# Kernel tuning notes

Hardware: AMD Instinct MI355X
Metric: run time of the kernel (lower is better)

The kernel has to match this reference:

```python
import jax, jax.numpy as jnp
import numpy as np

NEG = jnp.float32(-1e9)


def setup_inputs() -> dict:
    key = jax.random.key(0)
    ks = jax.random.split(key, 8)
    B, S, D = 8, 2048, 1024
    scale = 1.0 / np.sqrt(D)
    return {
        "xQ": jax.random.normal(ks[0], (B, S, D), jnp.float32),
        "xK": jax.random.normal(ks[1], (B, S, D), jnp.float32),
        "xV": jax.random.normal(ks[2], (B, S, D), jnp.float32),
        "padding_mask": jax.random.randint(ks[3], (B, S), 0, 2, jnp.int32),
        "casual_mask": jnp.ones((B, S), jnp.int32),
        "W_q": jax.random.normal(ks[4], (D, D), jnp.float32) * scale,
        "b_q": jnp.zeros((D,), jnp.float32),
        "W_k": jax.random.normal(ks[5], (D, D), jnp.float32) * scale,
        "b_k": jnp.zeros((D,), jnp.float32),
        "W_v": jax.random.normal(ks[6], (D, D), jnp.float32) * scale,
        "b_v": jnp.zeros((D,), jnp.float32),
    }


def reference(xQ, xK, xV, padding_mask, casual_mask, W_q, b_q, W_k, b_k, W_v, b_v):
    # Linear projections (torch nn.Linear: x @ W.T + b)
    Q = jnp.einsum('bsd,ed->bse', xQ, W_q) + b_q
    K = jnp.einsum('bsd,ed->bse', xK, W_k) + b_k
    V = jnp.einsum('bsd,ed->bse', xV, W_v) + b_v

    # Raw logits (note: original code applies NO 1/sqrt(dk) scaling)
    QKT = jnp.einsum('bqd,bkd->bqk', Q, K)  # [B, Sq, Sk]

    # Additive padding mask: -1e9 on padded key positions
    pad = jnp.where(padding_mask[:, None, :] == 0, NEG, jnp.float32(0.0))
    # Additive causal mask: -1e9 above the diagonal
    Sq, Sk = QKT.shape[1], QKT.shape[2]
    caus = jnp.where(
        jnp.tril(jnp.ones((Sq, Sk), dtype=bool)), jnp.float32(0.0), NEG
    )[None, :, :]
    QKT = QKT + pad + caus

    S = jax.nn.softmax(QKT, axis=-1)
    return jnp.einsum('bqk,bkd->bqd', S, V)
```

## Files before the change

### kernel.cpp

```cpp
#include <hip/hip_runtime.h>

typedef __attribute__((ext_vector_type(4))) float f4;
typedef __attribute__((ext_vector_type(4))) float f32x4;
typedef _Float16 half8 __attribute__((ext_vector_type(8)));

#define DEVI static __device__ __forceinline__

DEVI void gload_lds16(const void* g, void* l) {
  __builtin_amdgcn_global_load_lds(
      (const __attribute__((address_space(1))) void*)g,
      (__attribute__((address_space(3))) void*)l, 16, 0, 0);
}

DEVI unsigned int pack2(_Float16 a, _Float16 b) {
  unsigned short ua = __builtin_bit_cast(unsigned short, a);
  unsigned short ub = __builtin_bit_cast(unsigned short, b);
  return (unsigned int)ua | ((unsigned int)ub << 16);
}

DEVI int xcd_swz(int id, int n) {
  int q = n >> 3, r = n & 7;
  int x = id & 7, c = id >> 3;
  return (x < r ? x * (q + 1) : r * (q + 1) + (x - r) * q) + c;
}

#define FENCED_BARRIER()                \
  __builtin_amdgcn_sched_barrier(0);    \
  __builtin_amdgcn_s_barrier();         \
  __builtin_amdgcn_sched_barrier(0);

__global__ __launch_bounds__(256) void cvt_plain(const float* __restrict__ X,
                                                 _Float16* __restrict__ H,
                                                 int n4) {
  int i = blockIdx.x * 256 + threadIdx.x;
  const int stride = gridDim.x * 256;
  typedef _Float16 half4v __attribute__((ext_vector_type(4)));
  for (; i < n4; i += stride) {
    f4 x = ((const f4*)X)[i];
    half4v h;
#pragma unroll
    for (int j = 0; j < 4; ++j) h[j] = (_Float16)x[j];
    ((half4v*)H)[i] = h;
  }
}

template <int DUP>
__global__ __launch_bounds__(256) void cvt_wide(const float* __restrict__ X,
                                                _Float16* __restrict__ H,
                                                int n4) {
  int i = blockIdx.x * 256 + threadIdx.x;
  const int stride = gridDim.x * 256;
  for (; i < n4; i += stride) {
    f4 x = ((const f4*)X)[i];
    half8 o;
#pragma unroll
    for (int j = 0; j < 4; ++j) {
      _Float16 h = (_Float16)x[j];
      o[2 * j] = h;
      o[2 * j + 1] = DUP ? h : (_Float16)(x[j] - (float)h);
    }
    ((half8*)H)[i] = o;
  }
}

template <int AR, int BR>
DEVI void core(const _Float16* __restrict__ A0, const _Float16* __restrict__ B0,
               int lda, int ldb, int NS, _Float16* lds, f32x4 (&acc)[4][4]) {
  constexpr int WN = BR / 64;
  constexpr int ACH = AR * 32;
  constexpr int CHUNK = (AR + BR) * 32;
  const int tid = threadIdx.x;
  const int w = tid >> 6, lane = tid & 63;
  const int wm = w / WN, wn = w % WN;
  const int r16 = lane & 15, kg = lane >> 4;

  auto STAGE = [&](int t, int buf) {
    _Float16* base = lds + buf * CHUNK;
#pragma unroll
    for (int j = 0; j < AR / 128; ++j) {
      int g = j * 512 + tid;
      int row = g >> 2, c = g & 3;
      int cs = (c ^ (row >> 1)) & 3;
      gload_lds16(A0 + (size_t)row * lda + t * 32 + cs * 8,
                  base + (j * 512 + w * 64) * 8);
    }
    _Float16* bb = base + ACH;
#pragma unroll
    for (int j = 0; j < BR / 128; ++j) {
      int g = j * 512 + tid;
      int row = g >> 2, c = g & 3;
      int cs = (c ^ (row >> 1)) & 3;
      gload_lds16(B0 + (size_t)row * ldb + t * 32 + cs * 8,
                  bb + (j * 512 + w * 64) * 8);
    }
  };

  auto COMPUTE = [&](int buf) {
    const _Float16* la = lds + buf * CHUNK;
    const _Float16* lb = la + ACH;
    half8 a[4], b[4];
#pragma unroll
    for (int mi = 0; mi < 4; ++mi) {
      int row = wm * 64 + mi * 16 + r16;
      a[mi] = *(const half8*)(la + row * 32 + (((kg ^ (row >> 1)) & 3) * 8));
    }
#pragma unroll
    for (int ni = 0; ni < 4; ++ni) {
      int row = wn * 64 + ni * 16 + r16;
      b[ni] = *(const half8*)(lb + row * 32 + (((kg ^ (row >> 1)) & 3) * 8));
    }
    __builtin_amdgcn_s_setprio(1);
#pragma unroll
    for (int mi = 0; mi < 4; ++mi)
#pragma unroll
      for (int ni = 0; ni < 4; ++ni)
        acc[mi][ni] = __builtin_amdgcn_mfma_f32_16x16x32_f16(
            a[mi], b[ni], acc[mi][ni], 0, 0, 0);
    __builtin_amdgcn_s_setprio(0);
  };

  STAGE(0, 0);
  STAGE(1, 1);
  int t = 0;
  for (; t < NS - 1; ++t) {
    asm volatile("s_waitcnt vmcnt(3)" ::: "memory");
    FENCED_BARRIER();
    if (t + 2 < NS) STAGE(t + 2, (t + 2) % 3);
    COMPUTE(t % 3);
  }
  asm volatile("s_waitcnt vmcnt(0)" ::: "memory");
  FENCED_BARRIER();
  COMPUTE(t % 3);
}

DEVI void acc_zero(f32x4 (&acc)[4][4]) {
#pragma unroll
  for (int i = 0; i < 4; ++i)
#pragma unroll
    for (int j = 0; j < 4; ++j) acc[i][j] = (f32x4)0.0f;
}

template <int OUTMODE>
__global__ __launch_bounds__(512, 4) void proj_eng(
    const _Float16* __restrict__ Xi, const _Float16* __restrict__ Wd,
    const float* __restrict__ bias, unsigned int* __restrict__ OutU) {
  extern __shared__ _Float16 lds[];
  const int id = xcd_swz(blockIdx.x, gridDim.x);
  const int m0 = (id >> 3) * 256, n0 = (id & 7) * 128;
  f32x4 acc[4][4];
  acc_zero(acc);
  core<256, 128>(Xi + (size_t)m0 * 2048, Wd + (size_t)n0 * 2048, 2048, 2048,
                 64, lds, acc);
  const int tid = threadIdx.x;
  const int w = tid >> 6, lane = tid & 63;
  const int wm = w >> 1, wn = w & 1;
  const int r16 = lane & 15, kg = lane >> 4;
  float bcol[4];
#pragma unroll
  for (int ni = 0; ni < 4; ++ni) bcol[ni] = bias[n0 + wn * 64 + ni * 16 + r16];
#pragma unroll
  for (int mi = 0; mi < 4; ++mi) {
    int row = m0 + wm * 64 + mi * 16 + kg * 4;
#pragma unroll
    for (int ni = 0; ni < 4; ++ni) {
      int col = n0 + wn * 64 + ni * 16 + r16;
#pragma unroll
      for (int j = 0; j < 4; ++j) {
        float v = acc[mi][ni][j] + bcol[ni];
        _Float16 h = (_Float16)v;
        _Float16 x2 = OUTMODE ? h : (_Float16)(v - (float)h);
        OutU[(size_t)(row + j) * 1024 + col] = pack2(h, x2);
      }
    }
  }
}

__global__ __launch_bounds__(512, 4) void proj_eng_v(
    const _Float16* __restrict__ X, const _Float16* __restrict__ Wh,
    const float* __restrict__ bias, _Float16* __restrict__ Vt) {
  extern __shared__ _Float16 lds[];
  const int id = xcd_swz(blockIdx.x, gridDim.x);
  const int m0 = (id >> 3) * 256, n0 = (id & 7) * 128;
  f32x4 acc[4][4];
  acc_zero(acc);
  core<256, 128>(X + (size_t)m0 * 1024, Wh + (size_t)n0 * 1024, 1024, 1024, 32,
                 lds, acc);
  const int tid = threadIdx.x;
  const int w = tid >> 6, lane = tid & 63;
  const int wm = w >> 1, wn = w & 1;
  const int r16 = lane & 15, kg = lane >> 4;
  float bcol[4];
#pragma unroll
  for (int ni = 0; ni < 4; ++ni) bcol[ni] = bias[n0 + wn * 64 + ni * 16 + r16];
  __syncthreads();
  _Float16(*T)[256] = (_Float16(*)[256])lds;
#pragma unroll
  for (int mi = 0; mi < 4; ++mi) {
    int ml = wm * 64 + mi * 16 + kg * 4;
#pragma unroll
    for (int ni = 0; ni < 4; ++ni) {
      int nl = wn * 64 + ni * 16 + r16;
#pragma unroll
      for (int j = 0; j < 4; ++j)
        T[nl][ml + j] = (_Float16)(acc[mi][ni][j] + bcol[ni]);
    }
  }
  __syncthreads();
  const int b = m0 >> 11;
  const int s0 = m0 & 2047;
#pragma unroll
  for (int r = 0; r < 8; ++r) {
    int flat = tid + r * 512;
    int n = flat >> 5, c = flat & 31;
    half8 v = *(const half8*)&T[n][c * 8];
    *(half8*)(Vt + (size_t)b * (1024 * 2048) + (size_t)(n0 + n) * 2048 + s0 +
              c * 8) = v;
  }
}

__global__ __launch_bounds__(512, 4) void qk_eng(
    const _Float16* __restrict__ Qi, const _Float16* __restrict__ Kd,
    float* __restrict__ Lg, int bbase) {
  extern __shared__ _Float16 lds[];
  const int id = xcd_swz(blockIdx.x, gridDim.x);
  const int y = id / 72;
  int t = id % 72;
  int qt = 0, base = 0;
  while (t >= base + (qt >> 1) + 1) { base += (qt >> 1) + 1; ++qt; }
  const int kt = t - base;
  const int b = bbase + y;
  f32x4 acc[4][4];
  acc_zero(acc);
  core<128, 256>(Qi + ((size_t)b * 2048 + qt * 128) * 2048,
                 Kd + ((size_t)b * 2048 + kt * 256) * 2048, 2048, 2048, 64,
                 lds, acc);
  const int tid = threadIdx.x;
  const int w = tid >> 6, lane = tid & 63;
  const int wm = w >> 2, wn = w & 3;
  const int r16 = lane & 15, kg = lane >> 4;
  float* L = Lg + (size_t)y * (2048 * 2048);
#pragma unroll
  for (int mi = 0; mi < 4; ++mi) {
    int row = qt * 128 + wm * 64 + mi * 16 + kg * 4;
#pragma unroll
    for (int ni = 0; ni < 4; ++ni) {
      int col = kt * 256 + wn * 64 + ni * 16 + r16;
#pragma unroll
      for (int j = 0; j < 4; ++j)
        L[(size_t)(row + j) * 2048 + col] = acc[mi][ni][j];
    }
  }
}

__global__ __launch_bounds__(512, 4) void pv_eng(
    const float* __restrict__ Lg, const _Float16* __restrict__ Vt,
    float* __restrict__ Out, int bbase) {
  extern __shared__ _Float16 lds[];
  const int id = xcd_swz(blockIdx.x, gridDim.x);
  const int y = id >> 6;
  const int qt = (id & 63) >> 2, nt = id & 3;
  const int b = bbase + y;
  const _Float16* P = (const _Float16*)(Lg + (size_t)y * (2048 * 2048));
  f32x4 acc[4][4];
  acc_zero(acc);
  core<128, 256>(P + (size_t)(qt * 128) * 4096,
                 Vt + (size_t)b * (1024 * 2048) + (size_t)(nt * 256) * 2048,
                 4096, 2048, ((qt >> 1) + 1) * 8, lds, acc);
  const int tid = threadIdx.x;
  const int w = tid >> 6, lane = tid & 63;
  const int wm = w >> 2, wn = w & 3;
  const int r16 = lane & 15, kg = lane >> 4;
#pragma unroll
  for (int mi = 0; mi < 4; ++mi) {
    int row = qt * 128 + wm * 64 + mi * 16 + kg * 4;
#pragma unroll
    for (int ni = 0; ni < 4; ++ni) {
      int col = nt * 256 + wn * 64 + ni * 16 + r16;
#pragma unroll
      for (int j = 0; j < 4; ++j)
        Out[(size_t)(b * 2048 + row + j) * 1024 + col] = acc[mi][ni][j];
    }
  }
}

template <int OUTMODE>
__global__ __launch_bounds__(256) void proj_legacy(
    const float* __restrict__ X, const float* __restrict__ W,
    const float* __restrict__ bias, unsigned int* __restrict__ OutU) {
  __shared__ struct {
    float As[128][36];
    float Bs[128][36];
  } u;
  const int tid = threadIdx.x;
  const int lane = tid & 63, w = tid >> 6;
  const int wm = w >> 1, wn = w & 1;
  const int r16 = lane & 15, kg = lane >> 4;
  const int m0 = blockIdx.y * 128, n0 = blockIdx.x * 128;
  f32x4 acc[4][4];
  acc_zero(acc);
  f4 ra[4], rb[4];
  auto LOAD = [&](int kt) {
#pragma unroll
    for (int r = 0; r < 4; ++r) {
      int flat = tid + r * 256;
      int row = flat >> 3, c = flat & 7;
      ra[r] = *(const f4*)(X + (size_t)(m0 + row) * 1024 + kt * 32 + c * 4);
      rb[r] = *(const f4*)(W + (size_t)(n0 + row) * 1024 + kt * 32 + c * 4);
    }
  };
  LOAD(0);
  for (int kt = 0; kt < 32; ++kt) {
    __syncthreads();
#pragma unroll
    for (int r = 0; r < 4; ++r) {
      int flat = tid + r * 256;
      int row = flat >> 3, c = flat & 7;
      *(f4*)&u.As[row][c * 4] = ra[r];
      *(f4*)&u.Bs[row][c * 4] = rb[r];
    }
    __syncthreads();
    if (kt + 1 < 32) LOAD(kt + 1);
    half8 ah[4], al[4], bh[4];
#pragma unroll
    for (int mi = 0; mi < 4; ++mi) {
      const float* p = &u.As[wm * 64 + mi * 16 + r16][kg * 8];
      f4 x0 = *(const f4*)p, x1 = *(const f4*)(p + 4);
      half8 h, l;
#pragma unroll
      for (int j = 0; j < 4; ++j) {
        h[j] = (_Float16)x0[j];
        h[j + 4] = (_Float16)x1[j];
        l[j] = (_Float16)(x0[j] - (float)h[j]);
        l[j + 4] = (_Float16)(x1[j] - (float)h[j + 4]);
      }
      ah[mi] = h;
      al[mi] = l;
    }
#pragma unroll
    for (int ni = 0; ni < 4; ++ni) {
      const float* p = &u.Bs[wn * 64 + ni * 16 + r16][kg * 8];
      f4 x0 = *(const f4*)p, x1 = *(const f4*)(p + 4);
      half8 h;
#pragma unroll
      for (int j = 0; j < 4; ++j) {
        h[j] = (_Float16)x0[j];
        h[j + 4] = (_Float16)x1[j];
      }
      bh[ni] = h;
    }
#pragma unroll
    for (int mi = 0; mi < 4; ++mi)
#pragma unroll
      for (int ni = 0; ni < 4; ++ni) {
        acc[mi][ni] = __builtin_amdgcn_mfma_f32_16x16x32_f16(
            ah[mi], bh[ni], acc[mi][ni], 0, 0, 0);
        acc[mi][ni] = __builtin_amdgcn_mfma_f32_16x16x32_f16(
            al[mi], bh[ni], acc[mi][ni], 0, 0, 0);
      }
  }
  float bcol[4];
#pragma unroll
  for (int ni = 0; ni < 4; ++ni) bcol[ni] = bias[n0 + wn * 64 + ni * 16 + r16];
#pragma unroll
  for (int mi = 0; mi < 4; ++mi) {
    int row = m0 + wm * 64 + mi * 16 + kg * 4;
#pragma unroll
    for (int ni = 0; ni < 4; ++ni) {
      int col = n0 + wn * 64 + ni * 16 + r16;
#pragma unroll
      for (int j = 0; j < 4; ++j) {
        float v = acc[mi][ni][j] + bcol[ni];
        _Float16 h = (_Float16)v;
        _Float16 x2 = OUTMODE ? h : (_Float16)(v - (float)h);
        OutU[(size_t)(row + j) * 1024 + col] = pack2(h, x2);
      }
    }
  }
}

__global__ __launch_bounds__(256) void softmax_kernel(
    float* __restrict__ Lg, const int* __restrict__ pad, int bbase) {
  const int q = blockIdx.x;
  const int y = blockIdx.y;
  const int b = bbase + y;
  const int tid = threadIdx.x;
  float* row = Lg + (size_t)y * (2048 * 2048) + (size_t)q * 2048;
  _Float16* prow = (_Float16*)row;
  const int* pb = pad + (size_t)b * 2048;
  const int kend = ((q >> 8) + 1) << 8;
  float v[8];
  int nv = 0;
  float mx = -3.0e38f;
  for (int k = tid; k <= q; k += 256) {
    float l = row[k];
    if (pb[k] == 0) l += -1.0e9f;
    v[nv++] = l;
    mx = fmaxf(mx, l);
  }
  __shared__ float red[4];
  for (int o = 32; o; o >>= 1) mx = fmaxf(mx, __shfl_xor(mx, o));
  if ((tid & 63) == 0) red[tid >> 6] = mx;
  __syncthreads();
  mx = fmaxf(fmaxf(red[0], red[1]), fmaxf(red[2], red[3]));
  __syncthreads();
  float s = 0.f;
  for (int i = 0; i < nv; ++i) s += expf(v[i] - mx);
  for (int o = 32; o; o >>= 1) s += __shfl_xor(s, o);
  if ((tid & 63) == 0) red[tid >> 6] = s;
  __syncthreads();
  s = red[0] + red[1] + red[2] + red[3];
  const float inv = 1.0f / s;
  int i = 0;
  for (int k = tid; k <= q; k += 256) {
    prow[k] = (_Float16)(expf(v[i] - mx) * inv);
    ++i;
  }
  for (int k = q + 1 + tid; k < kend; k += 256) prow[k] = (_Float16)0.0f;
}

__global__ __launch_bounds__(512) void fix_f(const int* __restrict__ pad,
                                             int* __restrict__ fb) {
  const int b = threadIdx.x >> 6, k = threadIdx.x & 63;
  unsigned long long m = __ballot(pad[b * 2048 + k] != 0);
  if (k == 0) fb[b] = m ? (__ffsll((long long)m) - 1) : 64;
}

__global__ __launch_bounds__(256) void fix_qrow2(
    const float* __restrict__ xQ, const float* __restrict__ Wq,
    const float* __restrict__ bq, const int* __restrict__ fb,
    float* __restrict__ Qrow) {
  const int b = blockIdx.y;
  const int f = fb[b];
  const int tid = threadIdx.x;
  const int e = blockIdx.x * 16 + (tid >> 4);
  const int l16 = tid & 15;
  __shared__ float xq[1024];
  for (int q = 0; q < f; ++q) {
    *(f4*)&xq[tid * 4] = ((const f4*)(xQ + (size_t)(b * 2048 + q) * 1024))[tid];
    __syncthreads();
    float a = 0.f;
#pragma unroll
    for (int it = 0; it < 16; ++it) {
      int d = l16 * 4 + it * 64;
      f4 ww = *(const f4*)(Wq + (size_t)e * 1024 + d);
      a += xq[d] * ww[0] + xq[d + 1] * ww[1] + xq[d + 2] * ww[2] +
           xq[d + 3] * ww[3];
    }
    for (int o = 8; o; o >>= 1) a += __shfl_xor(a, o);
    if (l16 == 0) Qrow[((size_t)b * 64 + q) * 1024 + e] = a + bq[e];
    __syncthreads();
  }
}

__global__ __launch_bounds__(256) void fix_qb0(const float* __restrict__ bk,
                                               const int* __restrict__ fb,
                                               const float* __restrict__ Qrow,
                                               float* __restrict__ qb0) {
  const int q = blockIdx.x, b = blockIdx.y;
  if (q >= fb[b]) return;
  const int tid = threadIdx.x;
  const float* qr = Qrow + ((size_t)b * 64 + q) * 1024;
  float p = 0.f;
  for (int e = tid; e < 1024; e += 256) p += qr[e] * bk[e];
  __shared__ float red[4];
  for (int o = 32; o; o >>= 1) p += __shfl_xor(p, o);
  if ((tid & 63) == 0) red[tid >> 6] = p;
  __syncthreads();
  if (tid == 0) qb0[b * 64 + q] = red[0] + red[1] + red[2] + red[3];
}

__global__ __launch_bounds__(256) void fix_g2(const float* __restrict__ Wk,
                                              const int* __restrict__ fb,
                                              const float* __restrict__ Qrow,
                                              float* __restrict__ Gpart) {
  const int b = blockIdx.y;
  const int f = fb[b];
  const int tid = threadIdx.x;
  const int ddblk = blockIdx.x & 3, es = blockIdx.x >> 2;
  const int dd = ddblk * 256 + tid;
  __shared__ float qc[128];
  for (int q = 0; q < f; ++q) {
    if (tid < 32)
      *(f4*)&qc[tid * 4] =
          ((const f4*)(Qrow + ((size_t)b * 64 + q) * 1024 + es * 128))[tid];
    __syncthreads();
    float g = 0.f;
    for (int e = 0; e < 128; ++e)
      g += qc[e] * Wk[(size_t)(es * 128 + e) * 1024 + dd];
    Gpart[(((size_t)es * 8 + b) * 64 + q) * 1024 + dd] = g;
    __syncthreads();
  }
}

__global__ __launch_bounds__(256) void fix_logit2(
    const float* __restrict__ xK, const int* __restrict__ pad,
    const int* __restrict__ fb, const float* __restrict__ Gpart,
    const float* __restrict__ qb0, float* __restrict__ lrow) {
  const int b = blockIdx.y;
  const int f = fb[b];
  const int tid = threadIdx.x;
  const int k = blockIdx.x * 16 + (tid >> 4);
  const int l16 = tid & 15;
  __shared__ float Gs[1024];
  for (int q = 0; q < f; ++q) {
    f4 s = (f4)0.0f;
#pragma unroll
    for (int es = 0; es < 8; ++es)
      s += ((const f4*)(Gpart + (((size_t)es * 8 + b) * 64 + q) * 1024))[tid];
    *(f4*)&Gs[tid * 4] = s;
    __syncthreads();
    float a = 0.f;
#pragma unroll
    for (int it = 0; it < 16; ++it) {
      int d = l16 * 4 + it * 64;
      f4 x = *(const f4*)(xK + (size_t)(b * 2048 + k) * 1024 + d);
      a += x[0] * Gs[d] + x[1] * Gs[d + 1] + x[2] * Gs[d + 2] +
           x[3] * Gs[d + 3];
    }
    for (int o = 8; o; o >>= 1) a += __shfl_xor(a, o);
    if (l16 == 0) {
      float l = a + qb0[b * 64 + q];
      if (pad[b * 2048 + k] == 0) l += -1.0e9f;
      if (k > q) l += -1.0e9f;
      lrow[((size_t)b * 64 + q) * 2048 + k] = l;
    }
    __syncthreads();
  }
}

__global__ __launch_bounds__(256) void fix_sm(const int* __restrict__ fb,
                                              float* __restrict__ lrow,
                                              float* __restrict__ srow) {
  const int q = blockIdx.x, b = blockIdx.y;
  if (q >= fb[b]) return;
  const int tid = threadIdx.x;
  float* row = lrow + ((size_t)b * 64 + q) * 2048;
  float v[8];
  float mx = -3.0e38f;
#pragma unroll
  for (int i = 0; i < 8; ++i) {
    v[i] = row[tid + i * 256];
    mx = fmaxf(mx, v[i]);
  }
  __shared__ float red[4];
  for (int o = 32; o; o >>= 1) mx = fmaxf(mx, __shfl_xor(mx, o));
  if ((tid & 63) == 0) red[tid >> 6] = mx;
  __syncthreads();
  mx = fmaxf(fmaxf(red[0], red[1]), fmaxf(red[2], red[3]));
  __syncthreads();
  float s = 0.f;
#pragma unroll
  for (int i = 0; i < 8; ++i) {
    v[i] = expf(v[i] - mx);
    s += v[i];
  }
#pragma unroll
  for (int i = 0; i < 8; ++i) row[tid + i * 256] = v[i];
  for (int o = 32; o; o >>= 1) s += __shfl_xor(s, o);
  if ((tid & 63) == 0) red[tid >> 6] = s;
  __syncthreads();
  if (tid == 0) srow[b * 64 + q] = red[0] + red[1] + red[2] + red[3];
}

__global__ __launch_bounds__(256) void fix_pv2(
    const _Float16* __restrict__ Vt, const int* __restrict__ fb,
    const float* __restrict__ lrow, const float* __restrict__ srow,
    float* __restrict__ Out) {
  const int b = blockIdx.y;
  const int f = fb[b];
  const int tid = threadIdx.x;
  const int d = blockIdx.x * 16 + (tid >> 4);
  const int l16 = tid & 15;
  __shared__ float ps[2048];
  for (int q = 0; q < f; ++q) {
    const f4* src = (const f4*)(lrow + ((size_t)b * 64 + q) * 2048);
    *(f4*)&ps[tid * 8] = src[tid * 2];
    *(f4*)&ps[tid * 8 + 4] = src[tid * 2 + 1];
    __syncthreads();
    float o = 0.f;
#pragma unroll
    for (int it = 0; it < 16; ++it) {
      int k = l16 * 8 + it * 128;
      half8 vv = *(const half8*)(Vt + (size_t)b * (1024 * 2048) +
                                 (size_t)d * 2048 + k);
      o += (float)vv[0] * ps[k] + (float)vv[1] * ps[k + 1] +
           (float)vv[2] * ps[k + 2] + (float)vv[3] * ps[k + 3] +
           (float)vv[4] * ps[k + 4] + (float)vv[5] * ps[k + 5] +
           (float)vv[6] * ps[k + 6] + (float)vv[7] * ps[k + 7];
    }
    for (int of = 8; of; of >>= 1) o += __shfl_xor(o, of);
    if (l16 == 0)
      Out[(size_t)(b * 2048 + q) * 1024 + d] = o * (1.0f / srow[b * 64 + q]);
    __syncthreads();
  }
}

extern "C" void kernel_launch(void* const* d_in, const int* in_sizes, int n_in,
                              void* d_out, int out_size, void* d_ws,
                              size_t ws_size, hipStream_t stream) {
  const float* xQ = (const float*)d_in[0];
  const float* xK = (const float*)d_in[1];
  const float* xV = (const float*)d_in[2];
  const int* pad = (const int*)d_in[3];
  const float* Wq = (const float*)d_in[5];
  const float* bq = (const float*)d_in[6];
  const float* Wk = (const float*)d_in[7];
  const float* bk = (const float*)d_in[8];
  const float* Wv = (const float*)d_in[9];
  const float* bv = (const float*)d_in[10];
  float* Out = (float*)d_out;

  const size_t MB = (size_t)1 << 20;
  char* wsb = (char*)d_ws;
  _Float16* Qi = (_Float16*)(wsb);
  _Float16* Kd = (_Float16*)(wsb + 64 * MB);
  _Float16* Vt = (_Float16*)(wsb + 128 * MB);
  float* Lg = (float*)(wsb + 160 * MB);

  size_t avail = (ws_size > 160 * MB) ? ws_size - 160 * MB : 0;
  int G = (int)(avail / (16 * MB));
  if (G > 8) G = 8;
  if (G < 1) G = 1;

  const int SMEM = 73728;
  (void)hipFuncSetAttribute((const void*)&proj_eng<0>,
                            hipFuncAttributeMaxDynamicSharedMemorySize, SMEM);
  (void)hipFuncSetAttribute((const void*)&proj_eng<1>,
                            hipFuncAttributeMaxDynamicSharedMemorySize, SMEM);
  (void)hipFuncSetAttribute((const void*)&proj_eng_v,
                            hipFuncAttributeMaxDynamicSharedMemorySize, SMEM);
  (void)hipFuncSetAttribute((const void*)&qk_eng,
                            hipFuncAttributeMaxDynamicSharedMemorySize, SMEM);
  (void)hipFuncSetAttribute((const void*)&pv_eng,
                            hipFuncAttributeMaxDynamicSharedMemorySize, SMEM);

  dim3 blk(256), eblk(512);
  const bool fast = (ws_size >= 228 * MB);

  {
    _Float16* sX = (_Float16*)(wsb);
    _Float16* sW = (_Float16*)(wsb + 32 * MB);
    cvt_plain<<<dim3(2048), blk, 0, stream>>>(xV, sX, 4194304);
    cvt_plain<<<dim3(1024), blk, 0, stream>>>(Wv, sW, 262144);
    proj_eng_v<<<dim3(512), eblk, SMEM, stream>>>(sX, sW, bv, Vt);
  }
  if (fast) {
    _Float16* XiK = (_Float16*)(wsb);
    _Float16* WdK = (_Float16*)(wsb + 160 * MB);
    cvt_wide<0><<<dim3(2048), blk, 0, stream>>>(xK, XiK, 4194304);
    cvt_wide<1><<<dim3(1024), blk, 0, stream>>>(Wk, WdK, 262144);
    proj_eng<1><<<dim3(512), eblk, SMEM, stream>>>(XiK, WdK, bk,
                                                   (unsigned int*)Kd);
    _Float16* XiQ = (_Float16*)(wsb + 160 * MB);
    _Float16* WdQ = (_Float16*)(wsb + 224 * MB);
    cvt_wide<0><<<dim3(2048), blk, 0, stream>>>(xQ, XiQ, 4194304);
    cvt_wide<1><<<dim3(1024), blk, 0, stream>>>(Wq, WdQ, 262144);
    proj_eng<0><<<dim3(512), eblk, SMEM, stream>>>(XiQ, WdQ, bq,
                                                   (unsigned int*)Qi);
  } else {
    proj_legacy<1><<<dim3(8, 128), blk, 0, stream>>>(xK, Wk, bk,
                                                     (unsigned int*)Kd);
    proj_legacy<0><<<dim3(8, 128), blk, 0, stream>>>(xQ, Wq, bq,
                                                     (unsigned int*)Qi);
  }

  for (int bbase = 0; bbase < 8; bbase += G) {
    int nb = (8 - bbase < G) ? (8 - bbase) : G;
    qk_eng<<<dim3(72 * nb), eblk, SMEM, stream>>>(Qi, Kd, Lg, bbase);
    softmax_kernel<<<dim3(2048, nb), blk, 0, stream>>>(Lg, pad, bbase);
    pv_eng<<<dim3(64 * nb), eblk, SMEM, stream>>>(Lg, Vt, Out, bbase);
  }

  int* fb = (int*)(wsb);
  float* qb0 = (float*)(wsb + 4 * 1024);
  float* srow = (float*)(wsb + 8 * 1024);
  float* Qrow = (float*)(wsb + 1 * MB);
  float* Gpart = (float*)(wsb + 4 * MB);
  float* lrow = (float*)(wsb + 20 * MB);

  fix_f<<<dim3(1), dim3(512), 0, stream>>>(pad, fb);
  fix_qrow2<<<dim3(64, 8), blk, 0, stream>>>(xQ, Wq, bq, fb, Qrow);
  fix_qb0<<<dim3(64, 8), blk, 0, stream>>>(bk, fb, Qrow, qb0);
  fix_g2<<<dim3(32, 8), blk, 0, stream>>>(Wk, fb, Qrow, Gpart);
  fix_logit2<<<dim3(128, 8), blk, 0, stream>>>(xK, pad, fb, Gpart, qb0, lrow);
  fix_sm<<<dim3(64, 8), blk, 0, stream>>>(fb, lrow, srow);
  fix_pv2<<<dim3(64, 8), blk, 0, stream>>>(Vt, fb, lrow, srow, Out);
}
```

Baseline: 603.3 us.

## Fuse fp32-to-fp16 activation conversion into projections and split Q/K hi-lo buffers

Projection kernels now read fp32 activations directly, convert them to fp16 in registers and write them to LDS, which removes the separate activation conversion passes and their workspace traffic. Weights are split into separate hi and lo fp16 arrays that are multiplied separately. Q is likewise stored as separate hi and lo arrays, while K is stored hi-only. The QK and PV kernels are retiled into smaller tiles (64-row Q tiles, 128-column PV tiles) with more blocks for better load balance across the causal triangle. The legacy fallback path is removed. Risks include lower occupancy (launch bounds 512,2), a serialised register-staged A pipeline in the projections, and the inner products now running a different number of split-precision MFMA passes.

```diff
diff --git a/kernel.cpp b/kernel.cpp
--- a/kernel.cpp
+++ b/kernel.cpp
@@ -12,12 +12,6 @@
       (__attribute__((address_space(3))) void*)l, 16, 0, 0);
 }
 
-DEVI unsigned int pack2(_Float16 a, _Float16 b) {
-  unsigned short ua = __builtin_bit_cast(unsigned short, a);
-  unsigned short ub = __builtin_bit_cast(unsigned short, b);
-  return (unsigned int)ua | ((unsigned int)ub << 16);
-}
-
 DEVI int xcd_swz(int id, int n) {
   int q = n >> 3, r = n & 7;
   int x = id & 7, c = id >> 3;
@@ -28,6 +22,8 @@
   __builtin_amdgcn_sched_barrier(0);    \
   __builtin_amdgcn_s_barrier();         \
   __builtin_amdgcn_sched_barrier(0);
+
+#define SWZ(kgv, rowv) ((((kgv) ^ ((rowv) >> 1)) & 3) * 8)
 
 __global__ __launch_bounds__(256) void cvt_plain(const float* __restrict__ X,
                                                  _Float16* __restrict__ H,
@@ -44,207 +40,291 @@
   }
 }
 
-template <int DUP>
-__global__ __launch_bounds__(256) void cvt_wide(const float* __restrict__ X,
-                                                _Float16* __restrict__ H,
-                                                int n4) {
+__global__ __launch_bounds__(256) void cvt_split(const float* __restrict__ X,
+                                                 _Float16* __restrict__ H,
+                                                 _Float16* __restrict__ L,
+                                                 int n4) {
   int i = blockIdx.x * 256 + threadIdx.x;
   const int stride = gridDim.x * 256;
+  typedef _Float16 half4v __attribute__((ext_vector_type(4)));
   for (; i < n4; i += stride) {
     f4 x = ((const f4*)X)[i];
-    half8 o;
+    half4v h, l;
 #pragma unroll
     for (int j = 0; j < 4; ++j) {
-      _Float16 h = (_Float16)x[j];
-      o[2 * j] = h;
-      o[2 * j + 1] = DUP ? h : (_Float16)(x[j] - (float)h);
-    }
-    ((half8*)H)[i] = o;
-  }
-}
-
-template <int AR, int BR>
-DEVI void core(const _Float16* __restrict__ A0, const _Float16* __restrict__ B0,
-               int lda, int ldb, int NS, _Float16* lds, f32x4 (&acc)[4][4]) {
-  constexpr int WN = BR / 64;
-  constexpr int ACH = AR * 32;
-  constexpr int CHUNK = (AR + BR) * 32;
+      h[j] = (_Float16)x[j];
+      l[j] = (_Float16)(x[j] - (float)h[j]);
+    }
+    ((half4v*)H)[i] = h;
+    ((half4v*)L)[i] = l;
+  }
+}
+
+DEVI void acc_zero44(f32x4 (&acc)[4][4]) {
+#pragma unroll
+  for (int i = 0; i < 4; ++i)
+#pragma unroll
+    for (int j = 0; j < 4; ++j) acc[i][j] = (f32x4)0.0f;
+}
+DEVI void acc_zero42(f32x4 (&acc)[4][2]) {
+#pragma unroll
+  for (int i = 0; i < 4; ++i)
+#pragma unroll
+    for (int j = 0; j < 2; ++j) acc[i][j] = (f32x4)0.0f;
+}
+
+template <int WSPLIT, int OUTMODE>
+__global__ __launch_bounds__(512, 2) void proj_fused(
+    const float* __restrict__ X, const _Float16* __restrict__ Wh,
+    const _Float16* __restrict__ Wl, const float* __restrict__ bias,
+    _Float16* __restrict__ OutHi, _Float16* __restrict__ OutLo,
+    _Float16* __restrict__ VtOut) {
+  extern __shared__ _Float16 lds[];
+  constexpr int ACH = 256 * 32;
+  constexpr int BCH = 128 * 32;
+  constexpr int CHUNK = ACH + BCH * (1 + WSPLIT);
+  const int id = xcd_swz(blockIdx.x, gridDim.x);
+  const int m0 = (id >> 3) * 256, n0 = (id & 7) * 128;
+  const float* A = X + (size_t)m0 * 1024;
+  const _Float16* B0 = Wh + (size_t)n0 * 1024;
+  const _Float16* B1 = Wl + (size_t)n0 * 1024;
   const int tid = threadIdx.x;
   const int w = tid >> 6, lane = tid & 63;
-  const int wm = w / WN, wn = w % WN;
+  const int wm = w >> 1, wn = w & 1;
   const int r16 = lane & 15, kg = lane >> 4;
-
-  auto STAGE = [&](int t, int buf) {
-    _Float16* base = lds + buf * CHUNK;
-#pragma unroll
-    for (int j = 0; j < AR / 128; ++j) {
-      int g = j * 512 + tid;
+  f32x4 acc[4][4];
+  acc_zero44(acc);
+  f4 ra[4];
+
+  auto ALOAD = [&](int t) {
+#pragma unroll
+    for (int j = 0; j < 2; ++j) {
+      int g = tid + j * 512;
       int row = g >> 2, c = g & 3;
-      int cs = (c ^ (row >> 1)) & 3;
-      gload_lds16(A0 + (size_t)row * lda + t * 32 + cs * 8,
-                  base + (j * 512 + w * 64) * 8);
-    }
-    _Float16* bb = base + ACH;
-#pragma unroll
-    for (int j = 0; j < BR / 128; ++j) {
-      int g = j * 512 + tid;
+      const float* src = A + (size_t)row * 1024 + t * 32 + c * 8;
+      ra[2 * j] = *(const f4*)src;
+      ra[2 * j + 1] = *(const f4*)(src + 4);
+    }
+  };
+  auto AWRITE = [&](int buf) {
+    _Float16* ab = lds + buf * CHUNK;
+#pragma unroll
+    for (int j = 0; j < 2; ++j) {
+      int g = tid + j * 512;
       int row = g >> 2, c = g & 3;
-      int cs = (c ^ (row >> 1)) & 3;
-      gload_lds16(B0 + (size_t)row * ldb + t * 32 + cs * 8,
-                  bb + (j * 512 + w * 64) * 8);
+      half8 h;
+#pragma unroll
+      for (int e = 0; e < 4; ++e) {
+        h[e] = (_Float16)ra[2 * j][e];
+        h[e + 4] = (_Float16)ra[2 * j + 1][e];
+      }
+      *(half8*)(ab + (size_t)row * 32 + SWZ(c, row)) = h;
     }
   };
-
+  auto WLOAD = [&](int t, int buf) {
+    _Float16* bb = lds + buf * CHUNK + ACH;
+    int row = tid >> 2, c = tid & 3;
+    int cs = (c ^ (row >> 1)) & 3;
+    gload_lds16(B0 + (size_t)row * 1024 + t * 32 + cs * 8, bb + tid * 8);
+    if (WSPLIT)
+      gload_lds16(B1 + (size_t)row * 1024 + t * 32 + cs * 8,
+                  bb + BCH + tid * 8);
+  };
   auto COMPUTE = [&](int buf) {
     const _Float16* la = lds + buf * CHUNK;
     const _Float16* lb = la + ACH;
-    half8 a[4], b[4];
+    half8 a[4], b0f[4], b1f[4];
 #pragma unroll
     for (int mi = 0; mi < 4; ++mi) {
       int row = wm * 64 + mi * 16 + r16;
-      a[mi] = *(const half8*)(la + row * 32 + (((kg ^ (row >> 1)) & 3) * 8));
+      a[mi] = *(const half8*)(la + row * 32 + SWZ(kg, row));
     }
 #pragma unroll
     for (int ni = 0; ni < 4; ++ni) {
       int row = wn * 64 + ni * 16 + r16;
-      b[ni] = *(const half8*)(lb + row * 32 + (((kg ^ (row >> 1)) & 3) * 8));
+      int off = row * 32 + SWZ(kg, row);
+      b0f[ni] = *(const half8*)(lb + off);
+      if (WSPLIT) b1f[ni] = *(const half8*)(lb + BCH + off);
     }
     __builtin_amdgcn_s_setprio(1);
 #pragma unroll
     for (int mi = 0; mi < 4; ++mi)
 #pragma unroll
-      for (int ni = 0; ni < 4; ++ni)
+      for (int ni = 0; ni < 4; ++ni) {
         acc[mi][ni] = __builtin_amdgcn_mfma_f32_16x16x32_f16(
-            a[mi], b[ni], acc[mi][ni], 0, 0, 0);
+            a[mi], b0f[ni], acc[mi][ni], 0, 0, 0);
+        if (WSPLIT)
+          acc[mi][ni] = __builtin_amdgcn_mfma_f32_16x16x32_f16(
+              a[mi], b1f[ni], acc[mi][ni], 0, 0, 0);
+      }
     __builtin_amdgcn_s_setprio(0);
   };
 
+  const int NS = 32;
+  WLOAD(0, 0);
+  ALOAD(0);
+  asm volatile("s_waitcnt vmcnt(0)" ::: "memory");
+  __builtin_amdgcn_sched_barrier(0);
+  AWRITE(0);
+  asm volatile("s_waitcnt lgkmcnt(0)" ::: "memory");
+  FENCED_BARRIER();
+  for (int t = 0; t < NS; ++t) {
+    if (t + 1 < NS) {
+      WLOAD(t + 1, (t + 1) & 1);
+      ALOAD(t + 1);
+    }
+    COMPUTE(t & 1);
+    if (t + 1 < NS) {
+      asm volatile("s_waitcnt vmcnt(0)" ::: "memory");
+      __builtin_amdgcn_sched_barrier(0);
+      AWRITE((t + 1) & 1);
+      asm volatile("s_waitcnt lgkmcnt(0)" ::: "memory");
+      FENCED_BARRIER();
+    }
+  }
+
+  float bcol[4];
+#pragma unroll
+  for (int ni = 0; ni < 4; ++ni) bcol[ni] = bias[n0 + wn * 64 + ni * 16 + r16];
+
+  if (OUTMODE != 2) {
+#pragma unroll
+    for (int mi = 0; mi < 4; ++mi) {
+      int row = m0 + wm * 64 + mi * 16 + kg * 4;
+#pragma unroll
+      for (int ni = 0; ni < 4; ++ni) {
+        int col = n0 + wn * 64 + ni * 16 + r16;
+#pragma unroll
+        for (int j = 0; j < 4; ++j) {
+          float v = acc[mi][ni][j] + bcol[ni];
+          _Float16 h = (_Float16)v;
+          OutHi[(size_t)(row + j) * 1024 + col] = h;
+          if (OUTMODE == 0)
+            OutLo[(size_t)(row + j) * 1024 + col] = (_Float16)(v - (float)h);
+        }
+      }
+    }
+  } else {
+    __syncthreads();
+    _Float16(*T)[256] = (_Float16(*)[256])lds;
+#pragma unroll
+    for (int mi = 0; mi < 4; ++mi) {
+      int ml = wm * 64 + mi * 16 + kg * 4;
+#pragma unroll
+      for (int ni = 0; ni < 4; ++ni) {
+        int nl = wn * 64 + ni * 16 + r16;
+#pragma unroll
+        for (int j = 0; j < 4; ++j)
+          T[nl][ml + j] = (_Float16)(acc[mi][ni][j] + bcol[ni]);
+      }
+    }
+    __syncthreads();
+    const int b = m0 >> 11;
+    const int s0 = m0 & 2047;
+#pragma unroll
+    for (int r = 0; r < 8; ++r) {
+      int flat = tid + r * 512;
+      int n = flat >> 5, c = flat & 31;
+      half8 v = *(const half8*)&T[n][c * 8];
+      *(half8*)(VtOut + (size_t)b * (1024 * 2048) + (size_t)(n0 + n) * 2048 +
+                s0 + c * 8) = v;
+    }
+  }
+}
+
+__global__ __launch_bounds__(512, 4) void qk_eng(
+    const _Float16* __restrict__ Qh, const _Float16* __restrict__ Ql,
+    const _Float16* __restrict__ Kh, float* __restrict__ Lg, int bbase) {
+  extern __shared__ _Float16 lds[];
+  constexpr int CHUNK = 12288;
+  const int id = xcd_swz(blockIdx.x, gridDim.x);
+  const int y = id / 144;
+  int t = id % 144;
+  int g4 = 0, base = 0;
+  while (t >= base + (g4 + 1) * 4) { base += (g4 + 1) * 4; ++g4; }
+  const int rem = t - base;
+  const int qt = g4 * 4 + rem / (g4 + 1);
+  const int kt = rem % (g4 + 1);
+  const int b = bbase + y;
+  const size_t boff = (size_t)b * (2048 * 1024);
+  const _Float16* A0 = Qh + boff + (size_t)(qt * 64) * 1024;
+  const _Float16* A1 = Ql + boff + (size_t)(qt * 64) * 1024;
+  const _Float16* B0 = Kh + boff + (size_t)(kt * 256) * 1024;
+  const int tid = threadIdx.x;
+  const int w = tid >> 6, lane = tid & 63;
+  const int r16 = lane & 15, kg = lane >> 4;
+  const int wn = w;
+  f32x4 acc[4][2];
+  acc_zero42(acc);
+
+  auto STAGE = [&](int t_, int buf) {
+    _Float16* base_ = lds + buf * CHUNK;
+    {
+      int g = tid & 255;
+      int row = g >> 2, c = g & 3;
+      int cs = (c ^ (row >> 1)) & 3;
+      const _Float16* src = (tid < 256) ? A0 : A1;
+      _Float16* dst = base_ + ((tid < 256) ? 0 : 2048);
+      gload_lds16(src + (size_t)row * 1024 + t_ * 32 + cs * 8, dst + g * 8);
+    }
+#pragma unroll
+    for (int j = 0; j < 2; ++j) {
+      int g = tid + j * 512;
+      int row = g >> 2, c = g & 3;
+      int cs = (c ^ (row >> 1)) & 3;
+      gload_lds16(B0 + (size_t)row * 1024 + t_ * 32 + cs * 8,
+                  base_ + 4096 + g * 8);
+    }
+  };
+  auto COMPUTE = [&](int buf) {
+    const _Float16* la = lds + buf * CHUNK;
+    half8 a0[4], a1[4], bf[2];
+#pragma unroll
+    for (int mi = 0; mi < 4; ++mi) {
+      int row = mi * 16 + r16;
+      int off = row * 32 + SWZ(kg, row);
+      a0[mi] = *(const half8*)(la + off);
+      a1[mi] = *(const half8*)(la + 2048 + off);
+    }
+#pragma unroll
+    for (int ni = 0; ni < 2; ++ni) {
+      int row = wn * 32 + ni * 16 + r16;
+      bf[ni] = *(const half8*)(la + 4096 + row * 32 + SWZ(kg, row));
+    }
+    __builtin_amdgcn_s_setprio(1);
+#pragma unroll
+    for (int mi = 0; mi < 4; ++mi)
+#pragma unroll
+      for (int ni = 0; ni < 2; ++ni) {
+        acc[mi][ni] = __builtin_amdgcn_mfma_f32_16x16x32_f16(
+            a0[mi], bf[ni], acc[mi][ni], 0, 0, 0);
+        acc[mi][ni] = __builtin_amdgcn_mfma_f32_16x16x32_f16(
+            a1[mi], bf[ni], acc[mi][ni], 0, 0, 0);
+      }
+    __builtin_amdgcn_s_setprio(0);
+  };
+
+  const int NS = 32;
   STAGE(0, 0);
   STAGE(1, 1);
-  int t = 0;
-  for (; t < NS - 1; ++t) {
+  int tt = 0;
+  for (; tt < NS - 1; ++tt) {
     asm volatile("s_waitcnt vmcnt(3)" ::: "memory");
     FENCED_BARRIER();
-    if (t + 2 < NS) STAGE(t + 2, (t + 2) % 3);
-    COMPUTE(t % 3);
+    if (tt + 2 < NS) STAGE(tt + 2, (tt + 2) % 3);
+    COMPUTE(tt % 3);
   }
   asm volatile("s_waitcnt vmcnt(0)" ::: "memory");
   FENCED_BARRIER();
-  COMPUTE(t % 3);
-}
-
-DEVI void acc_zero(f32x4 (&acc)[4][4]) {
-#pragma unroll
-  for (int i = 0; i < 4; ++i)
-#pragma unroll
-    for (int j = 0; j < 4; ++j) acc[i][j] = (f32x4)0.0f;
-}
-
-template <int OUTMODE>
-__global__ __launch_bounds__(512, 4) void proj_eng(
-    const _Float16* __restrict__ Xi, const _Float16* __restrict__ Wd,
-    const float* __restrict__ bias, unsigned int* __restrict__ OutU) {
-  extern __shared__ _Float16 lds[];
-  const int id = xcd_swz(blockIdx.x, gridDim.x);
-  const int m0 = (id >> 3) * 256, n0 = (id & 7) * 128;
-  f32x4 acc[4][4];
-  acc_zero(acc);
-  core<256, 128>(Xi + (size_t)m0 * 2048, Wd + (size_t)n0 * 2048, 2048, 2048,
-                 64, lds, acc);
-  const int tid = threadIdx.x;
-  const int w = tid >> 6, lane = tid & 63;
-  const int wm = w >> 1, wn = w & 1;
-  const int r16 = lane & 15, kg = lane >> 4;
-  float bcol[4];
-#pragma unroll
-  for (int ni = 0; ni < 4; ++ni) bcol[ni] = bias[n0 + wn * 64 + ni * 16 + r16];
+  COMPUTE(tt % 3);
+
+  float* L = Lg + (size_t)y * (2048 * 2048);
 #pragma unroll
   for (int mi = 0; mi < 4; ++mi) {
-    int row = m0 + wm * 64 + mi * 16 + kg * 4;
-#pragma unroll
-    for (int ni = 0; ni < 4; ++ni) {
-      int col = n0 + wn * 64 + ni * 16 + r16;
-#pragma unroll
-      for (int j = 0; j < 4; ++j) {
-        float v = acc[mi][ni][j] + bcol[ni];
-        _Float16 h = (_Float16)v;
-        _Float16 x2 = OUTMODE ? h : (_Float16)(v - (float)h);
-        OutU[(size_t)(row + j) * 1024 + col] = pack2(h, x2);
-      }
-    }
-  }
-}
-
-__global__ __launch_bounds__(512, 4) void proj_eng_v(
-    const _Float16* __restrict__ X, const _Float16* __restrict__ Wh,
-    const float* __restrict__ bias, _Float16* __restrict__ Vt) {
-  extern __shared__ _Float16 lds[];
-  const int id = xcd_swz(blockIdx.x, gridDim.x);
-  const int m0 = (id >> 3) * 256, n0 = (id & 7) * 128;
-  f32x4 acc[4][4];
-  acc_zero(acc);
-  core<256, 128>(X + (size_t)m0 * 1024, Wh + (size_t)n0 * 1024, 1024, 1024, 32,
-                 lds, acc);
-  const int tid = threadIdx.x;
-  const int w = tid >> 6, lane = tid & 63;
-  const int wm = w >> 1, wn = w & 1;
-  const int r16 = lane & 15, kg = lane >> 4;
-  float bcol[4];
-#pragma unroll
-  for (int ni = 0; ni < 4; ++ni) bcol[ni] = bias[n0 + wn * 64 + ni * 16 + r16];
-  __syncthreads();
-  _Float16(*T)[256] = (_Float16(*)[256])lds;
-#pragma unroll
-  for (int mi = 0; mi < 4; ++mi) {
-    int ml = wm * 64 + mi * 16 + kg * 4;
-#pragma unroll
-    for (int ni = 0; ni < 4; ++ni) {
-      int nl = wn * 64 + ni * 16 + r16;
-#pragma unroll
-      for (int j = 0; j < 4; ++j)
-        T[nl][ml + j] = (_Float16)(acc[mi][ni][j] + bcol[ni]);
-    }
-  }
-  __syncthreads();
-  const int b = m0 >> 11;
-  const int s0 = m0 & 2047;
-#pragma unroll
-  for (int r = 0; r < 8; ++r) {
-    int flat = tid + r * 512;
-    int n = flat >> 5, c = flat & 31;
-    half8 v = *(const half8*)&T[n][c * 8];
-    *(half8*)(Vt + (size_t)b * (1024 * 2048) + (size_t)(n0 + n) * 2048 + s0 +
-              c * 8) = v;
-  }
-}
-
-__global__ __launch_bounds__(512, 4) void qk_eng(
-    const _Float16* __restrict__ Qi, const _Float16* __restrict__ Kd,
-    float* __restrict__ Lg, int bbase) {
-  extern __shared__ _Float16 lds[];
-  const int id = xcd_swz(blockIdx.x, gridDim.x);
-  const int y = id / 72;
-  int t = id % 72;
-  int qt = 0, base = 0;
-  while (t >= base + (qt >> 1) + 1) { base += (qt >> 1) + 1; ++qt; }
-  const int kt = t - base;
-  const int b = bbase + y;
-  f32x4 acc[4][4];
-  acc_zero(acc);
-  core<128, 256>(Qi + ((size_t)b * 2048 + qt * 128) * 2048,
-                 Kd + ((size_t)b * 2048 + kt * 256) * 2048, 2048, 2048, 64,
-                 lds, acc);
-  const int tid = threadIdx.x;
-  const int w = tid >> 6, lane = tid & 63;
-  const int wm = w >> 2, wn = w & 3;
-  const int r16 = lane & 15, kg = lane >> 4;
-  float* L = Lg + (size_t)y * (2048 * 2048);
-#pragma unroll
-  for (int mi = 0; mi < 4; ++mi) {
-    int row = qt * 128 + wm * 64 + mi * 16 + kg * 4;
-#pragma unroll
-    for (int ni = 0; ni < 4; ++ni) {
-      int col = kt * 256 + wn * 64 + ni * 16 + r16;
+    int row = qt * 64 + mi * 16 + kg * 4;
+#pragma unroll
+    for (int ni = 0; ni < 2; ++ni) {
+      int col = kt * 256 + wn * 32 + ni * 16 + r16;
 #pragma unroll
       for (int j = 0; j < 4; ++j)
         L[(size_t)(row + j) * 2048 + col] = acc[mi][ni][j];
@@ -256,124 +336,78 @@
     const float* __restrict__ Lg, const _Float16* __restrict__ Vt,
     float* __restrict__ Out, int bbase) {
   extern __shared__ _Float16 lds[];
+  constexpr int CHUNK = 8192;
   const int id = xcd_swz(blockIdx.x, gridDim.x);
-  const int y = id >> 6;
-  const int qt = (id & 63) >> 2, nt = id & 3;
+  const int y = id >> 7;
+  const int qt = (id & 127) >> 3, nt = id & 7;
   const int b = bbase + y;
   const _Float16* P = (const _Float16*)(Lg + (size_t)y * (2048 * 2048));
-  f32x4 acc[4][4];
-  acc_zero(acc);
-  core<128, 256>(P + (size_t)(qt * 128) * 4096,
-                 Vt + (size_t)b * (1024 * 2048) + (size_t)(nt * 256) * 2048,
-                 4096, 2048, ((qt >> 1) + 1) * 8, lds, acc);
+  const _Float16* A0 = P + (size_t)(qt * 128) * 4096;
+  const _Float16* B0 =
+      Vt + (size_t)b * (1024 * 2048) + (size_t)(nt * 128) * 2048;
+  const int NS = (qt + 1) * 4;
   const int tid = threadIdx.x;
   const int w = tid >> 6, lane = tid & 63;
   const int wm = w >> 2, wn = w & 3;
   const int r16 = lane & 15, kg = lane >> 4;
+  f32x4 acc[4][2];
+  acc_zero42(acc);
+
+  auto STAGE = [&](int t_, int buf) {
+    _Float16* base_ = lds + buf * CHUNK;
+    {
+      int row = tid >> 2, c = tid & 3;
+      int cs = (c ^ (row >> 1)) & 3;
+      gload_lds16(A0 + (size_t)row * 4096 + t_ * 32 + cs * 8, base_ + tid * 8);
+      gload_lds16(B0 + (size_t)row * 2048 + t_ * 32 + cs * 8,
+                  base_ + 4096 + tid * 8);
+    }
+  };
+  auto COMPUTE = [&](int buf) {
+    const _Float16* la = lds + buf * CHUNK;
+    half8 a[4], bf[2];
+#pragma unroll
+    for (int mi = 0; mi < 4; ++mi) {
+      int row = wm * 64 + mi * 16 + r16;
+      a[mi] = *(const half8*)(la + row * 32 + SWZ(kg, row));
+    }
+#pragma unroll
+    for (int ni = 0; ni < 2; ++ni) {
+      int row = wn * 32 + ni * 16 + r16;
+      bf[ni] = *(const half8*)(la + 4096 + row * 32 + SWZ(kg, row));
+    }
+    __builtin_amdgcn_s_setprio(1);
+#pragma unroll
+    for (int mi = 0; mi < 4; ++mi)
+#pragma unroll
+      for (int ni = 0; ni < 2; ++ni)
+        acc[mi][ni] = __builtin_amdgcn_mfma_f32_16x16x32_f16(
+            a[mi], bf[ni], acc[mi][ni], 0, 0, 0);
+    __builtin_amdgcn_s_setprio(0);
+  };
+
+  STAGE(0, 0);
+  STAGE(1, 1);
+  int tt = 0;
+  for (; tt < NS - 1; ++tt) {
+    asm volatile("s_waitcnt vmcnt(2)" ::: "memory");
+    FENCED_BARRIER();
+    if (tt + 2 < NS) STAGE(tt + 2, (tt + 2) % 3);
+    COMPUTE(tt % 3);
+  }
+  asm volatile("s_waitcnt vmcnt(0)" ::: "memory");
+  FENCED_BARRIER();
+  COMPUTE(tt % 3);
+
 #pragma unroll
   for (int mi = 0; mi < 4; ++mi) {
     int row = qt * 128 + wm * 64 + mi * 16 + kg * 4;
 #pragma unroll
-    for (int ni = 0; ni < 4; ++ni) {
-      int col = nt * 256 + wn * 64 + ni * 16 + r16;
+    for (int ni = 0; ni < 2; ++ni) {
+      int col = nt * 128 + wn * 32 + ni * 16 + r16;
 #pragma unroll
       for (int j = 0; j < 4; ++j)
         Out[(size_t)(b * 2048 + row + j) * 1024 + col] = acc[mi][ni][j];
-    }
-  }
-}
-
-template <int OUTMODE>
-__global__ __launch_bounds__(256) void proj_legacy(
-    const float* __restrict__ X, const float* __restrict__ W,
-    const float* __restrict__ bias, unsigned int* __restrict__ OutU) {
-  __shared__ struct {
-    float As[128][36];
-    float Bs[128][36];
-  } u;
-  const int tid = threadIdx.x;
-  const int lane = tid & 63, w = tid >> 6;
-  const int wm = w >> 1, wn = w & 1;
-  const int r16 = lane & 15, kg = lane >> 4;
-  const int m0 = blockIdx.y * 128, n0 = blockIdx.x * 128;
-  f32x4 acc[4][4];
-  acc_zero(acc);
-  f4 ra[4], rb[4];
-  auto LOAD = [&](int kt) {
-#pragma unroll
-    for (int r = 0; r < 4; ++r) {
-      int flat = tid + r * 256;
-      int row = flat >> 3, c = flat & 7;
-      ra[r] = *(const f4*)(X + (size_t)(m0 + row) * 1024 + kt * 32 + c * 4);
-      rb[r] = *(const f4*)(W + (size_t)(n0 + row) * 1024 + kt * 32 + c * 4);
-    }
-  };
-  LOAD(0);
-  for (int kt = 0; kt < 32; ++kt) {
-    __syncthreads();
-#pragma unroll
-    for (int r = 0; r < 4; ++r) {
-      int flat = tid + r * 256;
-      int row = flat >> 3, c = flat & 7;
-      *(f4*)&u.As[row][c * 4] = ra[r];
-      *(f4*)&u.Bs[row][c * 4] = rb[r];
-    }
-    __syncthreads();
-    if (kt + 1 < 32) LOAD(kt + 1);
-    half8 ah[4], al[4], bh[4];
-#pragma unroll
-    for (int mi = 0; mi < 4; ++mi) {
-      const float* p = &u.As[wm * 64 + mi * 16 + r16][kg * 8];
-      f4 x0 = *(const f4*)p, x1 = *(const f4*)(p + 4);
-      half8 h, l;
-#pragma unroll
-      for (int j = 0; j < 4; ++j) {
-        h[j] = (_Float16)x0[j];
-        h[j + 4] = (_Float16)x1[j];
-        l[j] = (_Float16)(x0[j] - (float)h[j]);
-        l[j + 4] = (_Float16)(x1[j] - (float)h[j + 4]);
-      }
-      ah[mi] = h;
-      al[mi] = l;
-    }
-#pragma unroll
-    for (int ni = 0; ni < 4; ++ni) {
-      const float* p = &u.Bs[wn * 64 + ni * 16 + r16][kg * 8];
-      f4 x0 = *(const f4*)p, x1 = *(const f4*)(p + 4);
-      half8 h;
-#pragma unroll
-      for (int j = 0; j < 4; ++j) {
-        h[j] = (_Float16)x0[j];
-        h[j + 4] = (_Float16)x1[j];
-      }
-      bh[ni] = h;
-    }
-#pragma unroll
-    for (int mi = 0; mi < 4; ++mi)
-#pragma unroll
-      for (int ni = 0; ni < 4; ++ni) {
-        acc[mi][ni] = __builtin_amdgcn_mfma_f32_16x16x32_f16(
-            ah[mi], bh[ni], acc[mi][ni], 0, 0, 0);
-        acc[mi][ni] = __builtin_amdgcn_mfma_f32_16x16x32_f16(
-            al[mi], bh[ni], acc[mi][ni], 0, 0, 0);
-      }
-  }
-  float bcol[4];
-#pragma unroll
-  for (int ni = 0; ni < 4; ++ni) bcol[ni] = bias[n0 + wn * 64 + ni * 16 + r16];
-#pragma unroll
-  for (int mi = 0; mi < 4; ++mi) {
-    int row = m0 + wm * 64 + mi * 16 + kg * 4;
-#pragma unroll
-    for (int ni = 0; ni < 4; ++ni) {
-      int col = n0 + wn * 64 + ni * 16 + r16;
-#pragma unroll
-      for (int j = 0; j < 4; ++j) {
-        float v = acc[mi][ni][j] + bcol[ni];
-        _Float16 h = (_Float16)v;
-        _Float16 x2 = OUTMODE ? h : (_Float16)(v - (float)h);
-        OutU[(size_t)(row + j) * 1024 + col] = pack2(h, x2);
-      }
     }
   }
 }
@@ -612,63 +646,56 @@
 
   const size_t MB = (size_t)1 << 20;
   char* wsb = (char*)d_ws;
-  _Float16* Qi = (_Float16*)(wsb);
-  _Float16* Kd = (_Float16*)(wsb + 64 * MB);
-  _Float16* Vt = (_Float16*)(wsb + 128 * MB);
-  float* Lg = (float*)(wsb + 160 * MB);
-
-  size_t avail = (ws_size > 160 * MB) ? ws_size - 160 * MB : 0;
+  _Float16* Qh = (_Float16*)(wsb);
+  _Float16* Ql = (_Float16*)(wsb + 32 * MB);
+  _Float16* Kh = (_Float16*)(wsb + 64 * MB);
+  _Float16* Vt = (_Float16*)(wsb + 96 * MB);
+  float* Lg = (float*)(wsb + 128 * MB);
+
+  size_t avail = (ws_size > 128 * MB) ? ws_size - 128 * MB : 0;
   int G = (int)(avail / (16 * MB));
   if (G > 8) G = 8;
   if (G < 1) G = 1;
 
-  const int SMEM = 73728;
-  (void)hipFuncSetAttribute((const void*)&proj_eng<0>,
-                            hipFuncAttributeMaxDynamicSharedMemorySize, SMEM);
-  (void)hipFuncSetAttribute((const void*)&proj_eng<1>,
-                            hipFuncAttributeMaxDynamicSharedMemorySize, SMEM);
-  (void)hipFuncSetAttribute((const void*)&proj_eng_v,
-                            hipFuncAttributeMaxDynamicSharedMemorySize, SMEM);
+  _Float16* Wqh = (_Float16*)(wsb + 128 * MB);
+  _Float16* Wql = (_Float16*)(wsb + 130 * MB);
+  _Float16* Wkh = (_Float16*)(wsb + 132 * MB);
+  _Float16* Wkl = (_Float16*)(wsb + 134 * MB);
+  _Float16* Wvh = (_Float16*)(wsb + 136 * MB);
+
+  const int SM_P = 65536;
+  const int SM_V = 65536;
+  const int SM_QK = 73728;
+  const int SM_PV = 49152;
+  (void)hipFuncSetAttribute((const void*)&proj_fused<1, 0>,
+                            hipFuncAttributeMaxDynamicSharedMemorySize, SM_P);
+  (void)hipFuncSetAttribute((const void*)&proj_fused<1, 1>,
+                            hipFuncAttributeMaxDynamicSharedMemorySize, SM_P);
+  (void)hipFuncSetAttribute((const void*)&proj_fused<0, 2>,
+                            hipFuncAttributeMaxDynamicSharedMemorySize, SM_V);
   (void)hipFuncSetAttribute((const void*)&qk_eng,
-                            hipFuncAttributeMaxDynamicSharedMemorySize, SMEM);
+                            hipFuncAttributeMaxDynamicSharedMemorySize, SM_QK);
   (void)hipFuncSetAttribute((const void*)&pv_eng,
-                            hipFuncAttributeMaxDynamicSharedMemorySize, SMEM);
+                            hipFuncAttributeMaxDynamicSharedMemorySize, SM_PV);
 
   dim3 blk(256), eblk(512);
-  const bool fast = (ws_size >= 228 * MB);
-
-  {
-    _Float16* sX = (_Float16*)(wsb);
-    _Float16* sW = (_Float16*)(wsb + 32 * MB);
-    cvt_plain<<<dim3(2048), blk, 0, stream>>>(xV, sX, 4194304);
-    cvt_plain<<<dim3(1024), blk, 0, stream>>>(Wv, sW, 262144);
-    proj_eng_v<<<dim3(512), eblk, SMEM, stream>>>(sX, sW, bv, Vt);
-  }
-  if (fast) {
-    _Float16* XiK = (_Float16*)(wsb);
-    _Float16* WdK = (_Float16*)(wsb + 160 * MB);
-    cvt_wide<0><<<dim3(2048), blk, 0, stream>>>(xK, XiK, 4194304);
-    cvt_wide<1><<<dim3(1024), blk, 0, stream>>>(Wk, WdK, 262144);
-    proj_eng<1><<<dim3(512), eblk, SMEM, stream>>>(XiK, WdK, bk,
-                                                   (unsigned int*)Kd);
-    _Float16* XiQ = (_Float16*)(wsb + 160 * MB);
-    _Float16* WdQ = (_Float16*)(wsb + 224 * MB);
-    cvt_wide<0><<<dim3(2048), blk, 0, stream>>>(xQ, XiQ, 4194304);
-    cvt_wide<1><<<dim3(1024), blk, 0, stream>>>(Wq, WdQ, 262144);
-    proj_eng<0><<<dim3(512), eblk, SMEM, stream>>>(XiQ, WdQ, bq,
-                                                   (unsigned int*)Qi);
-  } else {
-    proj_legacy<1><<<dim3(8, 128), blk, 0, stream>>>(xK, Wk, bk,
-                                                     (unsigned int*)Kd);
-    proj_legacy<0><<<dim3(8, 128), blk, 0, stream>>>(xQ, Wq, bq,
-                                                     (unsigned int*)Qi);
-  }
+
+  cvt_split<<<dim3(1024), blk, 0, stream>>>(Wq, Wqh, Wql, 262144);
+  cvt_split<<<dim3(1024), blk, 0, stream>>>(Wk, Wkh, Wkl, 262144);
+  cvt_plain<<<dim3(1024), blk, 0, stream>>>(Wv, Wvh, 262144);
+
+  proj_fused<0, 2><<<dim3(512), eblk, SM_V, stream>>>(xV, Wvh, Wvh, bv,
+                                                      nullptr, nullptr, Vt);
+  proj_fused<1, 1><<<dim3(512), eblk, SM_P, stream>>>(xK, Wkh, Wkl, bk, Kh,
+                                                      nullptr, nullptr);
+  proj_fused<1, 0><<<dim3(512), eblk, SM_P, stream>>>(xQ, Wqh, Wql, bq, Qh, Ql,
+                                                      nullptr);
 
   for (int bbase = 0; bbase < 8; bbase += G) {
     int nb = (8 - bbase < G) ? (8 - bbase) : G;
-    qk_eng<<<dim3(72 * nb), eblk, SMEM, stream>>>(Qi, Kd, Lg, bbase);
+    qk_eng<<<dim3(144 * nb), eblk, SM_QK, stream>>>(Qh, Ql, Kh, Lg, bbase);
     softmax_kernel<<<dim3(2048, nb), blk, 0, stream>>>(Lg, pad, bbase);
-    pv_eng<<<dim3(64 * nb), eblk, SMEM, stream>>>(Lg, Vt, Out, bbase);
+    pv_eng<<<dim3(128 * nb), eblk, SM_PV, stream>>>(Lg, Vt, Out, bbase);
   }
 
   int* fb = (int*)(wsb);
```

After: 547.5 us. 1.1x faster.
